# Kernel tuning notes

Hardware: AMD Instinct MI355X
Metric: run time of the kernel (lower is better)

The kernel has to match this reference:

```python
import jax, jax.numpy as jnp
import numpy as np

B, M, L, D = 64, 128, 20, 1024


def setup_inputs() -> dict:
    key = jax.random.key(0)
    ks = jax.random.split(key, 16)
    s = 0.05  # weight scale to keep LSTM gates out of saturation
    rn = lambda k, shape: jax.random.normal(k, shape, jnp.float32) * s
    return {
        'encoder_out': jax.random.normal(ks[0], (B, M + 1, D), jnp.float32),
        'obj_seq': jax.random.randint(ks[1], (B, L), 0, M),
        'att_mask': jnp.ones((B, M + 1), jnp.int32),
        'bos_w': rn(ks[2], (1, D)),
        'eos_w': rn(ks[3], (1, D)),
        'Wp': rn(ks[4], (D, D)), 'bp': jnp.zeros((D,), jnp.float32),
        'Wih1': rn(ks[5], (4 * D, 3 * D)), 'Whh1': rn(ks[6], (4 * D, D)),
        'bih1': jnp.zeros((4 * D,), jnp.float32), 'bhh1': jnp.zeros((4 * D,), jnp.float32),
        'Wih2': rn(ks[7], (4 * D, 2 * D)), 'Whh2': rn(ks[8], (4 * D, D)),
        'bih2': jnp.zeros((4 * D,), jnp.float32), 'bhh2': jnp.zeros((4 * D,), jnp.float32),
        'Wah': rn(ks[9], (D, D)), 'bah': jnp.zeros((D,), jnp.float32),
        'wa': rn(ks[10], (D,)), 'ba': jnp.zeros((1,), jnp.float32),
        'Wae': rn(ks[11], (D, D)), 'bae': jnp.zeros((D,), jnp.float32),
        'Woe': rn(ks[12], (D, D)), 'boe': jnp.zeros((D,), jnp.float32),
    }


def _lstm_cell(x, h, c, Wih, Whh, bih, bhh):
    # torch LSTMCell gate order: i, f, g, o
    g = x @ Wih.T + bih + h @ Whh.T + bhh
    i, f, gg, o = jnp.split(g, 4, axis=-1)
    c_new = jax.nn.sigmoid(f) * c + jax.nn.sigmoid(i) * jnp.tanh(gg)
    h_new = jax.nn.sigmoid(o) * jnp.tanh(c_new)
    return h_new, c_new


def _forward(encoder_out, obj_seq, att_mask, bos_w, eos_w, Wp, bp,
             Wih1, Whh1, bih1, bhh1, Wih2, Whh2, bih2, bhh2,
             Wah, bah, wa, ba, Wae, bae, Woe, boe):
    b, _, d = encoder_out.shape
    gv = encoder_out[:, 0, :]                      # [B, D]
    att_feats = encoder_out[:, 1:, :]              # [B, M, D]
    idx = jnp.broadcast_to(obj_seq[:, :, None], obj_seq.shape + (d,)).astype(jnp.int32)
    obj_feat = jnp.take_along_axis(att_feats, idx, axis=1)          # [B, L, D]
    bos = jnp.broadcast_to(bos_w, (b, 1, d))
    obj_feat = jnp.concatenate([bos, obj_feat], axis=1)             # [B, L+1, D]
    p_att = att_feats @ Wp.T + bp                  # [B, M, D]
    amask = att_mask[:, 1:]                        # [B, M]

    def attend(h1):
        dot = jnp.tanh(p_att + (h1 @ Wah.T + bah)[:, None, :])      # [B, M, D]
        score = dot @ wa + ba[0]                                    # [B, M]
        score = jnp.where(amask == 0, -1e9, score)
        alpha = jax.nn.softmax(score, axis=-1)
        return jnp.einsum('bm,bmd->bd', alpha, att_feats)

    def step(carry, x_t):
        h1, c1, h2, c2 = carry
        inp1 = jnp.concatenate([h2, gv, x_t], axis=-1)              # [B, 3D]
        h1, c1 = _lstm_cell(inp1, h1, c1, Wih1, Whh1, bih1, bhh1)
        att = attend(h1)
        inp2 = jnp.concatenate([att, h1], axis=-1)                  # [B, 2D]
        h2, c2 = _lstm_cell(inp2, h2, c2, Wih2, Whh2, bih2, bhh2)
        return (h1, c1, h2, c2), h2

    z = jnp.zeros((b, d), encoder_out.dtype)
    _, outs = jax.lax.scan(step, (z, z, z, z), jnp.swapaxes(obj_feat, 0, 1))
    outputs = jnp.swapaxes(outs, 0, 1)             # [B, L+1, D]

    # NCE branch (cfg.LOSSES.NCE.STOP_GRAD = True)
    nce_att = jax.lax.stop_gradient(att_feats)
    afe = nce_att @ Wae.T + bae
    eos = jnp.broadcast_to(eos_w, (b, 1, d))
    afe = jnp.concatenate([eos, afe], axis=1)      # [B, M+1, D]
    ofe = outputs @ Woe.T + boe                    # [B, L+1, D]
    nce_logit = jnp.einsum('bld,bmd->blm', ofe, afe)  # [B, L+1, M+1]
    return outputs, nce_logit


def reference(encoder_out, obj_seq, att_mask, bos_w, eos_w, Wp, bp,
              Wih1, Whh1, bih1, bhh1, Wih2, Whh2, bih2, bhh2,
              Wah, bah, wa, ba, Wae, bae, Woe, boe):
    return _forward(encoder_out, obj_seq, att_mask, bos_w, eos_w, Wp, bp,
                    Wih1, Whh1, bih1, bhh1, Wih2, Whh2, bih2, bhh2,
                    Wah, bah, wa, ba, Wae, bae, Woe, boe)
```

## Files before the change

### kernel.cpp

```cpp
#include <hip/hip_runtime.h>
#include <cmath>

typedef unsigned short u16;
typedef __attribute__((ext_vector_type(8))) short short8;
typedef __attribute__((ext_vector_type(4))) float floatx4;
typedef __attribute__((address_space(3))) unsigned int lds_u32;
typedef const __attribute__((address_space(1))) unsigned int glob_u32;

__device__ __forceinline__ u16 f2bf(float f) {
    unsigned u = __float_as_uint(f);
    unsigned r = u + 0x7fffu + ((u >> 16) & 1u);
    return (u16)(r >> 16);
}
__device__ __forceinline__ float bf2f(u16 h) { return __uint_as_float(((unsigned)h) << 16); }
__device__ __forceinline__ void split2(float x, u16& hi, u16& lo) {
    hi = f2bf(x);
    lo = f2bf(x - bf2f(hi));
}
__device__ __forceinline__ float sigm(float x) {
    x = fminf(fmaxf(x, -30.f), 30.f);
    return 1.0f / (1.0f + __expf(-x));
}
__device__ __forceinline__ float ftanh(float x) {
    x = fminf(fmaxf(x, -15.f), 15.f);
    float e = __expf(2.f * x);
    return (e - 1.f) / (e + 1.f);
}
__device__ __forceinline__ void gload16(const void* g, void* l) {
    __builtin_amdgcn_global_load_lds((glob_u32*)g, (lds_u32*)l, 16, 0, 0);
}

__global__ __launch_bounds__(256) void k_cvt(const float* __restrict__ s, u16* __restrict__ d, int n4) {
    int i = blockIdx.x * 256 + threadIdx.x;
    int stride = gridDim.x * 256;
    for (; i < n4; i += stride) {
        float4 v = ((const float4*)s)[i];
        ushort4 o;
        o.x = f2bf(v.x); o.y = f2bf(v.y); o.z = f2bf(v.z); o.w = f2bf(v.w);
        ((ushort4*)d)[i] = o;
    }
}

__global__ __launch_bounds__(256) void k_splitp(const float* __restrict__ s, u16* __restrict__ hi,
                                                u16* __restrict__ lo, int n4) {
    int i = blockIdx.x * 256 + threadIdx.x;
    int stride = gridDim.x * 256;
    for (; i < n4; i += stride) {
        float4 v = ((const float4*)s)[i];
        ushort4 h, l;
        split2(v.x, h.x, l.x); split2(v.y, h.y, l.y);
        split2(v.z, h.z, l.z); split2(v.w, h.w, l.w);
        ((ushort4*)hi)[i] = h;
        ((ushort4*)lo)[i] = l;
    }
}

__global__ __launch_bounds__(256) void k_build_w1cat(const float* __restrict__ Wih1, const float* __restrict__ Whh1,
                                                     u16* __restrict__ dh, u16* __restrict__ dl) {
    int row = blockIdx.x;
    int c = threadIdx.x * 8;
    const float* src = (c < 1024) ? (Wih1 + (size_t)row * 3072 + c) : (Whh1 + (size_t)row * 1024 + (c - 1024));
    short8 h, l;
#pragma unroll
    for (int j = 0; j < 8; ++j) { u16 hh, ll; split2(src[j], hh, ll); h[j] = (short)hh; l[j] = (short)ll; }
    *(short8*)(dh + (size_t)row * 2048 + c) = h;
    *(short8*)(dl + (size_t)row * 2048 + c) = l;
}

__global__ __launch_bounds__(384) void k_build_wcat2(const float* __restrict__ Wih2, const float* __restrict__ Whh2,
                                                     u16* __restrict__ dh, u16* __restrict__ dl) {
    int row = blockIdx.x;
    int c = threadIdx.x * 8;
    const float* src = (c < 2048) ? (Wih2 + (size_t)row * 2048 + c) : (Whh2 + (size_t)row * 1024 + (c - 2048));
    short8 h, l;
#pragma unroll
    for (int j = 0; j < 8; ++j) { u16 hh, ll; split2(src[j], hh, ll); h[j] = (short)hh; l[j] = (short)ll; }
    *(short8*)(dh + (size_t)row * 3072 + c) = h;
    *(short8*)(dl + (size_t)row * 3072 + c) = l;
}

__global__ __launch_bounds__(256) void k_build_wx1(const float* __restrict__ Wih1, u16* __restrict__ dh,
                                                   u16* __restrict__ dl) {
    int row = blockIdx.x;
    int c = threadIdx.x * 8;
    const float* src = Wih1 + (size_t)row * 3072 + 1024 + c;
    short8 h, l;
#pragma unroll
    for (int j = 0; j < 8; ++j) { u16 hh, ll; split2(src[j], hh, ll); h[j] = (short)hh; l[j] = (short)ll; }
    *(short8*)(dh + (size_t)row * 2048 + c) = h;
    *(short8*)(dl + (size_t)row * 2048 + c) = l;
}

__global__ __launch_bounds__(256) void k_build_xaug(const float* __restrict__ enc, const int* __restrict__ obj,
                                                    const float* __restrict__ bos_w, u16* __restrict__ dh,
                                                    u16* __restrict__ dl) {
    int b = blockIdx.x, t = blockIdx.y, tid = threadIdx.x;
    const float* gv = enc + (size_t)b * 129 * 1024;
    const float* xr;
    if (t == 0) xr = bos_w;
    else {
        int idx = obj[b * 20 + (t - 1)];
        idx = min(max(idx, 0), 127);
        xr = enc + ((size_t)b * 129 + 1 + idx) * 1024;
    }
    size_t rowoff = ((size_t)b * 21 + t) * 2048;
    float4 v0 = *(const float4*)(gv + tid * 4);
    float4 v1 = *(const float4*)(xr + tid * 4);
    ushort4 h0, l0, h1, l1;
    split2(v0.x, h0.x, l0.x); split2(v0.y, h0.y, l0.y); split2(v0.z, h0.z, l0.z); split2(v0.w, h0.w, l0.w);
    split2(v1.x, h1.x, l1.x); split2(v1.y, h1.y, l1.y); split2(v1.z, h1.z, l1.z); split2(v1.w, h1.w, l1.w);
    *(ushort4*)(dh + rowoff + tid * 4) = h0;
    *(ushort4*)(dl + rowoff + tid * 4) = l0;
    *(ushort4*)(dh + rowoff + 1024 + tid * 4) = h1;
    *(ushort4*)(dl + rowoff + 1024 + tid * 4) = l1;
}

template <int APASS, int BPASS, int AREMAP, bool BF16OUT>
__global__ __launch_bounds__(256)
void k_gemm3(const u16* __restrict__ Ah, const u16* __restrict__ Al, int lda,
             const u16* __restrict__ Wh, const u16* __restrict__ Wl, int ldw,
             const float* __restrict__ b1, const float* __restrict__ b2,
             void* __restrict__ Cout, int ldc, int Mrows, int K) {
    constexpr int NP = APASS + BPASS;
    __shared__ char lds[2][NP][8192];
    const int tid = threadIdx.x;
    const int lane = tid & 63;
    const int lr = lane & 15, lk = lane >> 4;
    const int m0 = blockIdx.y * 128, n0 = blockIdx.x * 128;
    const int wid = tid >> 6;
    const int wr = wid >> 1, wc = wid & 1;
    const int wbyte = (tid & 192) * 16;

    floatx4 acc[4][4] = {};
    const int nt = K >> 5;

    auto stage = [&](int bb, int kt) {
        int k0 = kt * 32;
#pragma unroll
        for (int i = 0; i < 2; ++i) {
            int p = i * 256 + tid;
            int s = p ^ ((p >> 2) & 3);
            int row = s >> 2, kc = s & 3;
            size_t aoff;
            int gm = m0 + row;
            if (AREMAP == 1) aoff = (((size_t)(gm >> 7)) * 129 + 1 + (gm & 127)) * 1024 + k0 + kc * 8;
            else {
                int cm = gm < Mrows ? gm : Mrows - 1;
                aoff = (size_t)cm * lda + k0 + kc * 8;
            }
            gload16(Ah + aoff, &lds[bb][0][i * 4096 + wbyte]);
            if constexpr (APASS == 2) gload16(Al + aoff, &lds[bb][1][i * 4096 + wbyte]);
            size_t woff = (size_t)(n0 + row) * ldw + k0 + kc * 8;
            gload16(Wh + woff, &lds[bb][APASS][i * 4096 + wbyte]);
            if constexpr (BPASS == 2) gload16(Wl + woff, &lds[bb][APASS + 1][i * 4096 + wbyte]);
        }
    };

    stage(0, 0);
    __syncthreads();
    for (int t = 0; t < nt; ++t) {
        int bb = t & 1;
        if (t + 1 < nt) stage(bb ^ 1, t + 1);
        short8 ah_[4], al_[4], bh_[4], bl_[4];
#pragma unroll
        for (int mi = 0; mi < 4; ++mi) {
            int row = wr * 64 + mi * 16 + lr;
            int slot = (row * 4 + (lk ^ (row & 3))) * 16;
            ah_[mi] = *(const short8*)&lds[bb][0][slot];
            if constexpr (APASS == 2) al_[mi] = *(const short8*)&lds[bb][1][slot];
        }
#pragma unroll
        for (int ni = 0; ni < 4; ++ni) {
            int row = wc * 64 + ni * 16 + lr;
            int slot = (row * 4 + (lk ^ (row & 3))) * 16;
            bh_[ni] = *(const short8*)&lds[bb][APASS][slot];
            if constexpr (BPASS == 2) bl_[ni] = *(const short8*)&lds[bb][APASS + 1][slot];
        }
#pragma unroll
        for (int mi = 0; mi < 4; ++mi)
#pragma unroll
            for (int ni = 0; ni < 4; ++ni) {
                acc[mi][ni] = __builtin_amdgcn_mfma_f32_16x16x32_bf16(ah_[mi], bh_[ni], acc[mi][ni], 0, 0, 0);
                if constexpr (BPASS == 2)
                    acc[mi][ni] = __builtin_amdgcn_mfma_f32_16x16x32_bf16(ah_[mi], bl_[ni], acc[mi][ni], 0, 0, 0);
                if constexpr (APASS == 2)
                    acc[mi][ni] = __builtin_amdgcn_mfma_f32_16x16x32_bf16(al_[mi], bh_[ni], acc[mi][ni], 0, 0, 0);
            }
        __syncthreads();
    }
#pragma unroll
    for (int mi = 0; mi < 4; ++mi) {
#pragma unroll
        for (int r = 0; r < 4; ++r) {
            int gm = m0 + wr * 64 + mi * 16 + lk * 4 + r;
            if (AREMAP == 0 && gm >= Mrows) continue;
#pragma unroll
            for (int ni = 0; ni < 4; ++ni) {
                int gn = n0 + wc * 64 + ni * 16 + lr;
                float v = acc[mi][ni][r];
                if (b1) v += b1[gn];
                if (b2) v += b2[gn];
                if (BF16OUT) ((u16*)Cout)[(size_t)gm * ldc + gn] = f2bf(v);
                else ((float*)Cout)[(size_t)gm * ldc + gn] = v;
            }
        }
    }
}

__global__ __launch_bounds__(256)
void k_gp3(const u16* __restrict__ Xh, const u16* __restrict__ Xl, int ldx,
           const u16* __restrict__ Wh, const u16* __restrict__ Wl, int ldw,
           int Klen, float* __restrict__ P, int Ntot) {
    __shared__ char lds[2][4][4096];
    const int tid = threadIdx.x, wid = tid >> 6, lane = tid & 63;
    const int lr = lane & 15, lk = lane >> 4;
    const int n0 = blockIdx.x * 64;
    const int koff = blockIdx.y * Klen;
    floatx4 acc[4] = {};
    const int nt = Klen >> 5;
    const int wbyte = (tid & 192) * 16;
    const int srow = tid >> 2, skc = (tid & 3) ^ (srow & 3);
    const size_t xoff = (size_t)srow * ldx + skc * 8;
    const size_t woff = (size_t)(n0 + srow) * ldw + skc * 8;

    auto stage = [&](int bb, int kt) {
        int k0 = koff + kt * 32;
        gload16(Xh + xoff + k0, &lds[bb][0][wbyte]);
        gload16(Xl + xoff + k0, &lds[bb][1][wbyte]);
        gload16(Wh + woff + k0, &lds[bb][2][wbyte]);
        gload16(Wl + woff + k0, &lds[bb][3][wbyte]);
    };

    stage(0, 0);
    __syncthreads();
    for (int t = 0; t < nt; ++t) {
        int bb = t & 1;
        if (t + 1 < nt) stage(bb ^ 1, t + 1);
        int arow = wid * 16 + lr;
        int aslot = (arow * 4 + (lk ^ (arow & 3))) * 16;
        short8 xh = *(const short8*)&lds[bb][0][aslot];
        short8 xl = *(const short8*)&lds[bb][1][aslot];
#pragma unroll
        for (int ni = 0; ni < 4; ++ni) {
            int brow = ni * 16 + lr;
            int bslot = (brow * 4 + (lk ^ (brow & 3))) * 16;
            short8 wh = *(const short8*)&lds[bb][2][bslot];
            short8 wl = *(const short8*)&lds[bb][3][bslot];
            acc[ni] = __builtin_amdgcn_mfma_f32_16x16x32_bf16(xh, wh, acc[ni], 0, 0, 0);
            acc[ni] = __builtin_amdgcn_mfma_f32_16x16x32_bf16(xh, wl, acc[ni], 0, 0, 0);
            acc[ni] = __builtin_amdgcn_mfma_f32_16x16x32_bf16(xl, wh, acc[ni], 0, 0, 0);
        }
        __syncthreads();
    }
    float* Pb = P + (size_t)blockIdx.y * 64 * Ntot;
#pragma unroll
    for (int ni = 0; ni < 4; ++ni)
#pragma unroll
        for (int r = 0; r < 4; ++r) {
            int b = wid * 16 + lk * 4 + r;
            Pb[(size_t)b * Ntot + n0 + ni * 16 + lr] = acc[ni][r];
        }
}

__global__ __launch_bounds__(256)
void k_finish(const float* __restrict__ P, int Ntot, const float* __restrict__ xcf,
              const float* __restrict__ b1, const float* __restrict__ b2,
              float* __restrict__ cst,
              u16* __restrict__ w1h, u16* __restrict__ w1l, int w1s,
              u16* __restrict__ w2h, u16* __restrict__ w2l, int w2s,
              float* __restrict__ outf, u16* __restrict__ oh) {
    int idx = blockIdx.x * 256 + threadIdx.x;
    int b = idx >> 10, d = idx & 1023;
    float g[4];
#pragma unroll
    for (int q = 0; q < 4; ++q) {
        int n = q * 1024 + d;
        float s = 0.f;
#pragma unroll
        for (int p = 0; p < 4; ++p) s += P[((size_t)p * 64 + b) * Ntot + n];
        if (xcf) s += xcf[(size_t)b * 21 * 4096 + n];
        if (b1) s += b1[n];
        if (b2) s += b2[n];
        g[q] = s;
    }
    float cp = cst[idx];
    float cn = sigm(g[1]) * cp + sigm(g[0]) * ftanh(g[2]);
    float hn = sigm(g[3]) * ftanh(cn);
    cst[idx] = cn;
    u16 hh, hl;
    split2(hn, hh, hl);
    w1h[b * w1s + d] = hh; w1l[b * w1s + d] = hl;
    w2h[b * w2s + d] = hh; w2l[b * w2s + d] = hl;
    if (outf) outf[(size_t)b * 21 * 1024 + d] = hn;
    if (oh) oh[(size_t)b * 21 * 1024 + d] = hh;
}

__global__ __launch_bounds__(256)
void k_score(const float* __restrict__ PAH, const float* __restrict__ bah,
             const float* __restrict__ wa, const float* __restrict__ ba,
             const float* __restrict__ Patt, const int* __restrict__ amask, float* __restrict__ SC) {
    int mc = blockIdx.x, b = blockIdx.y, tid = threadIdx.x;
    __shared__ float sah[1024], swa[1024];
    {
        int d = tid * 4;
        *(float4*)&swa[d] = *(const float4*)(wa + d);
        float4 s;
        float* sp = &s.x;
#pragma unroll
        for (int j = 0; j < 4; ++j) {
            float acc = bah[d + j];
            acc += PAH[(size_t)b * 1024 + d + j];
            acc += PAH[((size_t)64 + b) * 1024 + d + j];
            sp[j] = acc;
        }
        *(float4*)&sah[d] = s;
    }
    __syncthreads();
    int wv = tid >> 6, lane = tid & 63;
    float bav = ba[0];
    for (int j = 0; j < 8; ++j) {
        int m = mc * 32 + wv * 8 + j;
        const float* pr = Patt + ((size_t)(b * 128 + m)) * 1024;
        float part = 0.f;
#pragma unroll
        for (int c = 0; c < 4; ++c) {
            int d = c * 256 + lane * 4;
            float4 p4 = *(const float4*)(pr + d);
            float4 a4 = *(const float4*)&sah[d];
            float4 w4 = *(const float4*)&swa[d];
            part += ftanh(p4.x + a4.x) * w4.x + ftanh(p4.y + a4.y) * w4.y +
                    ftanh(p4.z + a4.z) * w4.z + ftanh(p4.w + a4.w) * w4.w;
        }
#pragma unroll
        for (int off = 32; off; off >>= 1) part += __shfl_down(part, off, 64);
        if (lane == 0) {
            float sc = part + bav;
            if (amask[b * 129 + 1 + m] == 0) sc = -1e9f;
            SC[b * 128 + m] = sc;
        }
    }
}

__global__ __launch_bounds__(256)
void k_attsum(const float* __restrict__ SC, const float* __restrict__ enc,
              u16* __restrict__ X2h, u16* __restrict__ X2l) {
    int dc = blockIdx.x, b = blockIdx.y, tid = threadIdx.x;
    __shared__ float salpha[128];
    __shared__ float sred[8];
    float sv = (tid < 128) ? SC[b * 128 + tid] : -1e30f;
    float mx = sv;
#pragma unroll
    for (int off = 32; off; off >>= 1) mx = fmaxf(mx, __shfl_down(mx, off, 64));
    if ((tid & 63) == 0) sred[tid >> 6] = mx;
    __syncthreads();
    float gmx = fmaxf(fmaxf(sred[0], sred[1]), fmaxf(sred[2], sred[3]));
    float ev = (tid < 128) ? __expf(sv - gmx) : 0.f;
    float s = ev;
#pragma unroll
    for (int off = 32; off; off >>= 1) s += __shfl_down(s, off, 64);
    if ((tid & 63) == 0) sred[4 + (tid >> 6)] = s;
    __syncthreads();
    float gsum = sred[4] + sred[5] + sred[6] + sred[7];
    if (tid < 128) salpha[tid] = ev / gsum;
    __syncthreads();
    int d = dc * 256 + tid;
    const float* base = enc + ((size_t)b * 129 + 1) * 1024 + d;
    float acc = 0.f;
#pragma unroll 8
    for (int m = 0; m < 128; ++m) acc += salpha[m] * base[(size_t)m * 1024];
    u16 hh, hl;
    split2(acc, hh, hl);
    X2h[b * 3072 + d] = hh;
    X2l[b * 3072 + d] = hl;
}

__global__ __launch_bounds__(256)
void k_nce(const float* __restrict__ OFE, const float* __restrict__ AFE,
           const float* __restrict__ eos_w, float* __restrict__ nce) {
    int l = blockIdx.x, b = blockIdx.y;
    __shared__ float sofe[1024];
    int tid = threadIdx.x;
    {
        float4 v = *(const float4*)(OFE + ((size_t)b * 21 + l) * 1024 + tid * 4);
        *(float4*)&sofe[tid * 4] = v;
    }
    __syncthreads();
    int w = tid >> 6, lane = tid & 63;
    float* outp = nce + ((size_t)b * 21 + l) * 129;
    for (int j = w; j < 129; j += 4) {
        const float* ar = (j == 0) ? eos_w : AFE + ((size_t)b * 128 + (j - 1)) * 1024;
        float part = 0.f;
#pragma unroll
        for (int c = 0; c < 4; ++c) {
            float4 a4 = *(const float4*)(ar + c * 256 + lane * 4);
            float4 o4 = *(const float4*)&sofe[c * 256 + lane * 4];
            part += a4.x * o4.x + a4.y * o4.y + a4.z * o4.z + a4.w * o4.w;
        }
#pragma unroll
        for (int off = 32; off; off >>= 1) part += __shfl_down(part, off, 64);
        if (lane == 0) outp[j] = part;
    }
}

extern "C" void kernel_launch(void* const* d_in, const int* in_sizes, int n_in,
                              void* d_out, int out_size, void* d_ws, size_t ws_size,
                              hipStream_t stream) {
    const float* enc  = (const float*)d_in[0];
    const int*   obj  = (const int*)d_in[1];
    const int*   amask= (const int*)d_in[2];
    const float* bosw = (const float*)d_in[3];
    const float* eosw = (const float*)d_in[4];
    const float* Wp   = (const float*)d_in[5];
    const float* bp   = (const float*)d_in[6];
    const float* Wih1 = (const float*)d_in[7];
    const float* Whh1 = (const float*)d_in[8];
    const float* bih1 = (const float*)d_in[9];
    const float* bhh1 = (const float*)d_in[10];
    const float* Wih2 = (const float*)d_in[11];
    const float* Whh2 = (const float*)d_in[12];
    const float* bih2 = (const float*)d_in[13];
    const float* bhh2 = (const float*)d_in[14];
    const float* Wah  = (const float*)d_in[15];
    const float* bah  = (const float*)d_in[16];
    const float* wa   = (const float*)d_in[17];
    const float* ba   = (const float*)d_in[18];
    const float* Wae  = (const float*)d_in[19];
    const float* bae  = (const float*)d_in[20];
    const float* Woe  = (const float*)d_in[21];
    const float* boe  = (const float*)d_in[22];

    float* outputs = (float*)d_out;
    float* nce     = outputs + (size_t)64 * 21 * 1024;

    char* wp = (char*)d_ws;
    auto alloc = [&](size_t bytes) -> char* { char* p = wp; wp += (bytes + 255) & ~(size_t)255; return p; };
    u16* encbf  = (u16*)alloc((size_t)64 * 129 * 1024 * 2);
    u16* Wph    = (u16*)alloc((size_t)1024 * 1024 * 2);
    u16* Wpl    = (u16*)alloc((size_t)1024 * 1024 * 2);
    u16* Xaugh  = (u16*)alloc((size_t)1344 * 2048 * 2);
    u16* Xaugl  = (u16*)alloc((size_t)1344 * 2048 * 2);
    u16* W1h    = (u16*)alloc((size_t)4096 * 2048 * 2);
    u16* W1l    = (u16*)alloc((size_t)4096 * 2048 * 2);
    u16* W2h    = (u16*)alloc((size_t)4096 * 3072 * 2);
    u16* W2l    = (u16*)alloc((size_t)4096 * 3072 * 2);
    u16* Wahh   = (u16*)alloc((size_t)1024 * 1024 * 2);
    u16* Wahl   = (u16*)alloc((size_t)1024 * 1024 * 2);
    u16* Waeh   = (u16*)alloc((size_t)1024 * 1024 * 2);
    u16* Wael   = (u16*)alloc((size_t)1024 * 1024 * 2);
    u16* Woeh   = (u16*)alloc((size_t)1024 * 1024 * 2);
    u16* Woel   = (u16*)alloc((size_t)1024 * 1024 * 2);
    char* region1 = alloc((size_t)2 * 4096 * 2048 * 2);
    u16* Wx1h = (u16*)region1;
    u16* Wx1l = (u16*)region1 + (size_t)4096 * 2048;
    float* AFE32 = (float*)region1;
    float* PattF = (float*)alloc((size_t)8192 * 1024 * 4);
    float* Xcf   = (float*)alloc((size_t)1344 * 4096 * 4);
    u16* Xouth   = (u16*)alloc((size_t)1344 * 1024 * 2);
    float* OFE32 = (float*)Xaugh;
    char* sp2 = (char*)encbf;
    auto alloc2 = [&](size_t bytes) -> char* { char* p = sp2; sp2 += (bytes + 255) & ~(size_t)255; return p; };
    float* P1  = (float*)alloc2((size_t)4 * 64 * 4096 * 4);
    float* P2  = (float*)alloc2((size_t)4 * 64 * 4096 * 4);
    float* PAH = (float*)alloc2((size_t)2 * 64 * 1024 * 4);
    u16* XHh   = (u16*)alloc2((size_t)64 * 2048 * 2);
    u16* XHl   = (u16*)alloc2((size_t)64 * 2048 * 2);
    u16* X2h   = (u16*)alloc2((size_t)64 * 3072 * 2);
    u16* X2l   = (u16*)alloc2((size_t)64 * 3072 * 2);
    float* c1  = (float*)alloc2((size_t)64 * 1024 * 4);
    float* c2  = (float*)alloc2((size_t)64 * 1024 * 4);
    float* SC  = (float*)alloc2((size_t)64 * 128 * 4);

    dim3 blk(256);
    k_cvt<<<2048, blk, 0, stream>>>(enc, encbf, 64 * 129 * 1024 / 4);
    k_splitp<<<1024, blk, 0, stream>>>(Wp, Wph, Wpl, 1024 * 1024 / 4);
    k_splitp<<<1024, blk, 0, stream>>>(Wah, Wahh, Wahl, 1024 * 1024 / 4);
    k_splitp<<<1024, blk, 0, stream>>>(Wae, Waeh, Wael, 1024 * 1024 / 4);
    k_splitp<<<1024, blk, 0, stream>>>(Woe, Woeh, Woel, 1024 * 1024 / 4);
    k_build_wx1<<<4096, blk, 0, stream>>>(Wih1, Wx1h, Wx1l);
    k_build_w1cat<<<4096, blk, 0, stream>>>(Wih1, Whh1, W1h, W1l);
    k_build_wcat2<<<4096, dim3(384), 0, stream>>>(Wih2, Whh2, W2h, W2l);
    k_build_xaug<<<dim3(64, 21), blk, 0, stream>>>(enc, obj, bosw, Xaugh, Xaugl);

    k_gemm3<1, 2, 1, false><<<dim3(8, 64), blk, 0, stream>>>(
        encbf, nullptr, 0, Wph, Wpl, 1024, bp, nullptr, PattF, 1024, 8192, 1024);
    k_gemm3<2, 2, 0, false><<<dim3(32, 11), blk, 0, stream>>>(
        Xaugh, Xaugl, 2048, Wx1h, Wx1l, 2048, bih1, bhh1, Xcf, 4096, 1344, 2048);
    k_gemm3<1, 2, 1, false><<<dim3(8, 64), blk, 0, stream>>>(
        encbf, nullptr, 0, Waeh, Wael, 1024, bae, nullptr, AFE32, 1024, 8192, 1024);

    hipMemsetAsync(XHh, 0, (size_t)64 * 2048 * 2, stream);
    hipMemsetAsync(XHl, 0, (size_t)64 * 2048 * 2, stream);
    hipMemsetAsync(X2h, 0, (size_t)64 * 3072 * 2, stream);
    hipMemsetAsync(X2l, 0, (size_t)64 * 3072 * 2, stream);
    hipMemsetAsync(c1, 0, (size_t)64 * 1024 * 4, stream);
    hipMemsetAsync(c2, 0, (size_t)64 * 1024 * 4, stream);

    for (int t = 0; t < 21; ++t) {
        k_gp3<<<dim3(64, 4), blk, 0, stream>>>(XHh, XHl, 2048, W1h, W1l, 2048, 512, P1, 4096);
        k_finish<<<256, blk, 0, stream>>>(P1, 4096, Xcf + (size_t)t * 4096, nullptr, nullptr,
                                          c1, XHh + 1024, XHl + 1024, 2048,
                                          X2h + 1024, X2l + 1024, 3072, nullptr, nullptr);
        k_gp3<<<dim3(16, 2), blk, 0, stream>>>(XHh + 1024, XHl + 1024, 2048, Wahh, Wahl, 1024, 512, PAH, 1024);
        k_score<<<dim3(4, 64), blk, 0, stream>>>(PAH, bah, wa, ba, PattF, amask, SC);
        k_attsum<<<dim3(4, 64), blk, 0, stream>>>(SC, enc, X2h, X2l);
        k_gp3<<<dim3(64, 4), blk, 0, stream>>>(X2h, X2l, 3072, W2h, W2l, 3072, 768, P2, 4096);
        k_finish<<<256, blk, 0, stream>>>(P2, 4096, nullptr, bih2, bhh2,
                                          c2, XHh, XHl, 2048,
                                          X2h + 2048, X2l + 2048, 3072,
                                          outputs + (size_t)t * 1024, Xouth + (size_t)t * 1024);
    }

    k_gemm3<1, 2, 0, false><<<dim3(8, 11), blk, 0, stream>>>(
        Xouth, nullptr, 1024, Woeh, Woel, 1024, boe, nullptr, OFE32, 1024, 1344, 1024);
    k_nce<<<dim3(21, 64), blk, 0, stream>>>(OFE32, AFE32, eosw, nce);
}
```

Measured before the change: 1.811 ms.

## Store attention features in bf16 and double split-K parallelism in recurrent GEMMs

```diff
diff --git a/kernel.cpp b/kernel.cpp
--- a/kernel.cpp
+++ b/kernel.cpp
@@ -39,6 +39,15 @@
         o.x = f2bf(v.x); o.y = f2bf(v.y); o.z = f2bf(v.z); o.w = f2bf(v.w);
         ((ushort4*)d)[i] = o;
     }
+}
+
+__global__ __launch_bounds__(256) void k_cvt_att(const float* __restrict__ enc, u16* __restrict__ dst) {
+    int m = blockIdx.x, b = blockIdx.y, tid = threadIdx.x;
+    const float* src = enc + ((size_t)b * 129 + 1 + m) * 1024;
+    float4 v = *(const float4*)(src + tid * 4);
+    ushort4 o;
+    o.x = f2bf(v.x); o.y = f2bf(v.y); o.z = f2bf(v.z); o.w = f2bf(v.w);
+    *(ushort4*)(dst + ((size_t)b * 128 + m) * 1024 + tid * 4) = o;
 }
 
 __global__ __launch_bounds__(256) void k_splitp(const float* __restrict__ s, u16* __restrict__ hi,
@@ -263,7 +272,7 @@
 }
 
 __global__ __launch_bounds__(256)
-void k_finish(const float* __restrict__ P, int Ntot, const float* __restrict__ xcf,
+void k_finish(const float* __restrict__ P, int Ntot, int nP, const float* __restrict__ xcf,
               const float* __restrict__ b1, const float* __restrict__ b2,
               float* __restrict__ cst,
               u16* __restrict__ w1h, u16* __restrict__ w1l, int w1s,
@@ -276,8 +285,7 @@
     for (int q = 0; q < 4; ++q) {
         int n = q * 1024 + d;
         float s = 0.f;
-#pragma unroll
-        for (int p = 0; p < 4; ++p) s += P[((size_t)p * 64 + b) * Ntot + n];
+        for (int p = 0; p < nP; ++p) s += P[((size_t)p * 64 + b) * Ntot + n];
         if (xcf) s += xcf[(size_t)b * 21 * 4096 + n];
         if (b1) s += b1[n];
         if (b2) s += b2[n];
@@ -298,7 +306,7 @@
 __global__ __launch_bounds__(256)
 void k_score(const float* __restrict__ PAH, const float* __restrict__ bah,
              const float* __restrict__ wa, const float* __restrict__ ba,
-             const float* __restrict__ Patt, const int* __restrict__ amask, float* __restrict__ SC) {
+             const u16* __restrict__ Patt, const int* __restrict__ amask, float* __restrict__ SC) {
     int mc = blockIdx.x, b = blockIdx.y, tid = threadIdx.x;
     __shared__ float sah[1024], swa[1024];
     {
@@ -309,8 +317,8 @@
 #pragma unroll
         for (int j = 0; j < 4; ++j) {
             float acc = bah[d + j];
-            acc += PAH[(size_t)b * 1024 + d + j];
-            acc += PAH[((size_t)64 + b) * 1024 + d + j];
+#pragma unroll
+            for (int p = 0; p < 4; ++p) acc += PAH[((size_t)p * 64 + b) * 1024 + d + j];
             sp[j] = acc;
         }
         *(float4*)&sah[d] = s;
@@ -320,16 +328,16 @@
     float bav = ba[0];
     for (int j = 0; j < 8; ++j) {
         int m = mc * 32 + wv * 8 + j;
-        const float* pr = Patt + ((size_t)(b * 128 + m)) * 1024;
+        const u16* pr = Patt + ((size_t)(b * 128 + m)) * 1024;
         float part = 0.f;
 #pragma unroll
         for (int c = 0; c < 4; ++c) {
             int d = c * 256 + lane * 4;
-            float4 p4 = *(const float4*)(pr + d);
+            ushort4 p4 = *(const ushort4*)(pr + d);
             float4 a4 = *(const float4*)&sah[d];
             float4 w4 = *(const float4*)&swa[d];
-            part += ftanh(p4.x + a4.x) * w4.x + ftanh(p4.y + a4.y) * w4.y +
-                    ftanh(p4.z + a4.z) * w4.z + ftanh(p4.w + a4.w) * w4.w;
+            part += ftanh(bf2f(p4.x) + a4.x) * w4.x + ftanh(bf2f(p4.y) + a4.y) * w4.y +
+                    ftanh(bf2f(p4.z) + a4.z) * w4.z + ftanh(bf2f(p4.w) + a4.w) * w4.w;
         }
 #pragma unroll
         for (int off = 32; off; off >>= 1) part += __shfl_down(part, off, 64);
@@ -342,7 +350,7 @@
 }
 
 __global__ __launch_bounds__(256)
-void k_attsum(const float* __restrict__ SC, const float* __restrict__ enc,
+void k_attsum(const float* __restrict__ SC, const u16* __restrict__ attf,
               u16* __restrict__ X2h, u16* __restrict__ X2l) {
     int dc = blockIdx.x, b = blockIdx.y, tid = threadIdx.x;
     __shared__ float salpha[128];
@@ -364,10 +372,10 @@
     if (tid < 128) salpha[tid] = ev / gsum;
     __syncthreads();
     int d = dc * 256 + tid;
-    const float* base = enc + ((size_t)b * 129 + 1) * 1024 + d;
+    const u16* base = attf + (size_t)b * 128 * 1024 + d;
     float acc = 0.f;
 #pragma unroll 8
-    for (int m = 0; m < 128; ++m) acc += salpha[m] * base[(size_t)m * 1024];
+    for (int m = 0; m < 128; ++m) acc += salpha[m] * bf2f(base[(size_t)m * 1024]);
     u16 hh, hl;
     split2(acc, hh, hl);
     X2h[b * 3072 + d] = hh;
@@ -453,15 +461,16 @@
     u16* Wx1h = (u16*)region1;
     u16* Wx1l = (u16*)region1 + (size_t)4096 * 2048;
     float* AFE32 = (float*)region1;
-    float* PattF = (float*)alloc((size_t)8192 * 1024 * 4);
+    u16* PattBf  = (u16*)alloc((size_t)8192 * 1024 * 2);
+    u16* attfbf  = (u16*)alloc((size_t)64 * 128 * 1024 * 2);
     float* Xcf   = (float*)alloc((size_t)1344 * 4096 * 4);
     u16* Xouth   = (u16*)alloc((size_t)1344 * 1024 * 2);
+    float* P2    = (float*)alloc((size_t)8 * 64 * 4096 * 4);
     float* OFE32 = (float*)Xaugh;
     char* sp2 = (char*)encbf;
     auto alloc2 = [&](size_t bytes) -> char* { char* p = sp2; sp2 += (bytes + 255) & ~(size_t)255; return p; };
-    float* P1  = (float*)alloc2((size_t)4 * 64 * 4096 * 4);
-    float* P2  = (float*)alloc2((size_t)4 * 64 * 4096 * 4);
-    float* PAH = (float*)alloc2((size_t)2 * 64 * 1024 * 4);
+    float* P1  = (float*)alloc2((size_t)8 * 64 * 4096 * 4);
+    float* PAH = (float*)alloc2((size_t)4 * 64 * 1024 * 4);
     u16* XHh   = (u16*)alloc2((size_t)64 * 2048 * 2);
     u16* XHl   = (u16*)alloc2((size_t)64 * 2048 * 2);
     u16* X2h   = (u16*)alloc2((size_t)64 * 3072 * 2);
@@ -472,6 +481,7 @@
 
     dim3 blk(256);
     k_cvt<<<2048, blk, 0, stream>>>(enc, encbf, 64 * 129 * 1024 / 4);
+    k_cvt_att<<<dim3(128, 64), blk, 0, stream>>>(enc, attfbf);
     k_splitp<<<1024, blk, 0, stream>>>(Wp, Wph, Wpl, 1024 * 1024 / 4);
     k_splitp<<<1024, blk, 0, stream>>>(Wah, Wahh, Wahl, 1024 * 1024 / 4);
     k_splitp<<<1024, blk, 0, stream>>>(Wae, Waeh, Wael, 1024 * 1024 / 4);
@@ -481,8 +491,8 @@
     k_build_wcat2<<<4096, dim3(384), 0, stream>>>(Wih2, Whh2, W2h, W2l);
     k_build_xaug<<<dim3(64, 21), blk, 0, stream>>>(enc, obj, bosw, Xaugh, Xaugl);
 
-    k_gemm3<1, 2, 1, false><<<dim3(8, 64), blk, 0, stream>>>(
-        encbf, nullptr, 0, Wph, Wpl, 1024, bp, nullptr, PattF, 1024, 8192, 1024);
+    k_gemm3<1, 2, 1, true><<<dim3(8, 64), blk, 0, stream>>>(
+        encbf, nullptr, 0, Wph, Wpl, 1024, bp, nullptr, PattBf, 1024, 8192, 1024);
     k_gemm3<2, 2, 0, false><<<dim3(32, 11), blk, 0, stream>>>(
         Xaugh, Xaugl, 2048, Wx1h, Wx1l, 2048, bih1, bhh1, Xcf, 4096, 1344, 2048);
     k_gemm3<1, 2, 1, false><<<dim3(8, 64), blk, 0, stream>>>(
@@ -496,15 +506,15 @@
     hipMemsetAsync(c2, 0, (size_t)64 * 1024 * 4, stream);
 
     for (int t = 0; t < 21; ++t) {
-        k_gp3<<<dim3(64, 4), blk, 0, stream>>>(XHh, XHl, 2048, W1h, W1l, 2048, 512, P1, 4096);
-        k_finish<<<256, blk, 0, stream>>>(P1, 4096, Xcf + (size_t)t * 4096, nullptr, nullptr,
+        k_gp3<<<dim3(64, 8), blk, 0, stream>>>(XHh, XHl, 2048, W1h, W1l, 2048, 256, P1, 4096);
+        k_finish<<<256, blk, 0, stream>>>(P1, 4096, 8, Xcf + (size_t)t * 4096, nullptr, nullptr,
                                           c1, XHh + 1024, XHl + 1024, 2048,
                                           X2h + 1024, X2l + 1024, 3072, nullptr, nullptr);
-        k_gp3<<<dim3(16, 2), blk, 0, stream>>>(XHh + 1024, XHl + 1024, 2048, Wahh, Wahl, 1024, 512, PAH, 1024);
-        k_score<<<dim3(4, 64), blk, 0, stream>>>(PAH, bah, wa, ba, PattF, amask, SC);
-        k_attsum<<<dim3(4, 64), blk, 0, stream>>>(SC, enc, X2h, X2l);
-        k_gp3<<<dim3(64, 4), blk, 0, stream>>>(X2h, X2l, 3072, W2h, W2l, 3072, 768, P2, 4096);
-        k_finish<<<256, blk, 0, stream>>>(P2, 4096, nullptr, bih2, bhh2,
+        k_gp3<<<dim3(16, 4), blk, 0, stream>>>(XHh + 1024, XHl + 1024, 2048, Wahh, Wahl, 1024, 256, PAH, 1024);
+        k_score<<<dim3(4, 64), blk, 0, stream>>>(PAH, bah, wa, ba, PattBf, amask, SC);
+        k_attsum<<<dim3(4, 64), blk, 0, stream>>>(SC, attfbf, X2h, X2l);
+        k_gp3<<<dim3(64, 8), blk, 0, stream>>>(X2h, X2l, 3072, W2h, W2l, 3072, 384, P2, 4096);
+        k_finish<<<256, blk, 0, stream>>>(P2, 4096, 8, nullptr, bih2, bhh2,
                                           c2, XHh, XHl, 2048,
                                           X2h + 2048, X2l + 2048, 3072,
                                           outputs + (size_t)t * 1024, Xouth + (size_t)t * 1024);
```

After: 1.899 ms. 1.05x slower.
